# Optimization experiments

Hardware: AMD Instinct MI355X
Metric: run time of the kernel (lower is better)

## Reference

```python
import jax, jax.numpy as jnp
import numpy as np

B = 16384          # batch
D = 1024           # input_size == hidden size of each block
L = 3              # number of hidden blocks (layer_configs)
H, Q = 4, 64       # num_heads, query_size
NKV, V = 128, 256  # num_key_values, value_size  (H*V == D for residual)
OUT = 256          # out_size
EPS = 1e-5


def layernorm(x, g, b):
    m = jnp.mean(x, axis=-1, keepdims=True)
    v = jnp.mean(jnp.square(x - m), axis=-1, keepdims=True)
    return (x - m) * jax.lax.rsqrt(v + EPS) * g + b


def setup_inputs() -> dict:
    key = jax.random.key(0)
    ks = jax.random.split(key, 16)
    scale = 1e-4  # module scales Linear / out_linear weights by 0.0001 at init
    return {
        "x": jax.random.normal(ks[0], (B, D), jnp.float32),
        # per-block Linear (stacked over L identical blocks)
        "W": jax.random.normal(ks[1], (L, D, D), jnp.float32) * scale / np.sqrt(D),
        "b": jax.random.normal(ks[2], (L, D), jnp.float32) * scale,
        # MemLayer params
        "Wq": jax.random.normal(ks[3], (L, H * Q, D), jnp.float32) / np.sqrt(D),
        "keys": jax.random.normal(ks[4], (L, NKV, Q), jnp.float32),
        "values": jax.random.normal(ks[5], (L, NKV, V), jnp.float32),
        "Wout": jax.random.normal(ks[6], (L, D, H * V), jnp.float32) * scale / np.sqrt(H * V),
        # per-block LayerNorm
        "ln_g": jnp.ones((L, D), jnp.float32),
        "ln_b": jnp.zeros((L, D), jnp.float32),
        # final head: Linear(sum(layer_configs)=L*D -> OUT), LayerNorm, Sigmoid
        "Wf": jax.random.normal(ks[7], (OUT, L * D), jnp.float32) * scale / np.sqrt(L * D),
        "bf": jax.random.normal(ks[8], (OUT,), jnp.float32) * scale,
        "lnf_g": jnp.ones((OUT,), jnp.float32),
        "lnf_b": jnp.zeros((OUT,), jnp.float32),
    }


def reference(x, W, b, Wq, keys, values, Wout, ln_g, ln_b, Wf, bf, lnf_g, lnf_b):
    # Dropout layers are identity at inference.
    inv_sqrt_q = 1.0 / np.sqrt(Q).astype(np.float32)
    outs = []
    h = x
    for i in range(L):
        # Linear + ReLU
        h = jax.nn.relu(h @ W[i].T + b[i])
        # MemLayer: scores = einsum('aib,ajb->aijb').sum(-1) == q @ k^T
        q = (h @ Wq[i].T).reshape(B, H, Q)
        scores = jnp.einsum('ahq,nq->ahn', q, keys[i]) * inv_sqrt_q  # (B,H,NKV)
        attn = jax.nn.softmax(scores, axis=-1)
        # einsum('aib,ajc->aijc').mean(axis=2) == attn.sum(-1)[:,:,None] * values.mean(0)
        s = jnp.sum(attn, axis=-1)              # (B,H)
        vmean = jnp.mean(values[i], axis=0)     # (V,)
        mem = (s[:, :, None] * vmean).reshape(B, H * V)
        h = mem @ Wout[i].T + h                 # out_linear + residual
        # LayerNorm (output collected for the final concat)
        h = layernorm(h, ln_g[i], ln_b[i])
        outs.append(h)
    z = jnp.concatenate(outs, axis=-1)          # (B, L*D)
    z = z @ Wf.T + bf
    z = layernorm(z, lnf_g, lnf_b)
    return jax.nn.sigmoid(z)
```

## Files before the change

### kernel.cpp

```cpp
#include <hip/hip_runtime.h>
#include <math.h>

#define EPS 1e-5f

constexpr int Bv   = 16384;
constexpr int Dv   = 1024;
constexpr int Lv   = 3;
constexpr int NKVv = 128;
constexpr int Vv   = 256;
constexpr int OUTv = 256;
constexpr int ZLD  = Lv * Dv;

typedef short bf16x8 __attribute__((ext_vector_type(8)));
typedef float f32x4  __attribute__((ext_vector_type(4)));

using gas_t = __attribute__((address_space(1))) const void;
using las_t = __attribute__((address_space(3))) void;
#define GLD_LDS16(gp, lp) \
    __builtin_amdgcn_global_load_lds((gas_t*)(gp), (las_t*)(lp), 16, 0, 0)

static __device__ __forceinline__ ushort f2bf(float f) {
    unsigned u = __float_as_uint(f);
    u = (u + 0x7fffu + ((u >> 16) & 1u)) >> 16;
    return (ushort)u;
}
static __device__ __forceinline__ ushort f2h(float f) {
    return __builtin_bit_cast(ushort, (_Float16)f);
}
static __device__ __forceinline__ float h2f(ushort u) {
    return (float)__builtin_bit_cast(_Float16, u);
}

__global__ void vmean_kernel(const float* __restrict__ values,
                             float* __restrict__ vmean) {
    const int i = blockIdx.x, t = threadIdx.x;
    const float* vals = values + (size_t)i * NKVv * Vv;
    float s = 0.f;
    for (int n = 0; n < NKVv; ++n) s += vals[n * Vv + t];
    vmean[i * Vv + t] = s * (1.0f / NKVv);
}

__global__ void cvec_kernel(const float* __restrict__ vmean,
                            const float* __restrict__ Wout,
                            float* __restrict__ cvec) {
    const int w = threadIdx.x >> 6, lane = threadIdx.x & 63;
    const int r = blockIdx.x * 8 + w;
    const int i = r >> 10;
    const float4 mv = *(const float4*)&vmean[i * Vv + lane * 4];
    const float* row = Wout + (size_t)r * 1024;
    float acc = 0.f;
#pragma unroll
    for (int c = 0; c < 4; ++c) {
        const float4 rv = *(const float4*)&row[c * 256 + lane * 4];
        acc += mv.x * rv.x + mv.y * rv.y + mv.z * rv.z + mv.w * rv.w;
    }
#pragma unroll
    for (int o = 1; o < 64; o <<= 1) acc += __shfl_xor(acc, o, 64);
    if (lane == 0) cvec[r] = acc;
}

__global__ void wprep(const float* __restrict__ W,
                      const float* __restrict__ lng,
                      const float* __restrict__ lnb,
                      ushort* __restrict__ Wb,
                      float* __restrict__ ub, float* __restrict__ vb) {
    __shared__ float rs[8];
    const int row = blockIdx.x;
    const int i = row >> 10, n = row & 1023;
    const int t = threadIdx.x, lane = t & 63, wv = t >> 6;
    const float* Wr = W + (size_t)row * 1024;
    const float4 w4 = *(const float4*)&Wr[t * 4];
    float4 g4 = make_float4(1.f, 1.f, 1.f, 1.f);
    float4 b4 = make_float4(0.f, 0.f, 0.f, 0.f);
    if (i > 0) {
        g4 = *(const float4*)&lng[(i - 1) * 1024 + t * 4];
        b4 = *(const float4*)&lnb[(i - 1) * 1024 + t * 4];
    }
    const float s0 = w4.x * g4.x, s1 = w4.y * g4.y, s2 = w4.z * g4.z, s3 = w4.w * g4.w;
    ushort4 o = {f2bf(s0), f2bf(s1), f2bf(s2), f2bf(s3)};
    *(ushort4*)&Wb[(size_t)row * 1024 + t * 4] = o;
    float su = s0 + s1 + s2 + s3;
    float sv = w4.x * b4.x + w4.y * b4.y + w4.z * b4.z + w4.w * b4.w;
#pragma unroll
    for (int d = 1; d < 64; d <<= 1) {
        su += __shfl_xor(su, d, 64);
        sv += __shfl_xor(sv, d, 64);
    }
    if (lane == 0) { rs[wv * 2] = su; rs[wv * 2 + 1] = sv; }
    __syncthreads();
    if (t == 0 && i > 0) {
        ub[(i - 1) * 1024 + n] = rs[0] + rs[2] + rs[4] + rs[6];
        vb[(i - 1) * 1024 + n] = rs[1] + rs[3] + rs[5] + rs[7];
    }
}

__global__ void wfprep(const float* __restrict__ Wf,
                       const float* __restrict__ lng,
                       const float* __restrict__ lnb,
                       ushort* __restrict__ Wfb,
                       float* __restrict__ uf, float* __restrict__ vf) {
    __shared__ float rs[8];
    const int bid = blockIdx.x;
    const int i = bid >> 8, n = bid & 255;
    const int t = threadIdx.x, lane = t & 63, wv = t >> 6;
    const size_t base = (size_t)n * ZLD + i * 1024 + t * 4;
    const float4 w4 = *(const float4*)&Wf[base];
    const float4 g4 = *(const float4*)&lng[i * 1024 + t * 4];
    const float4 b4 = *(const float4*)&lnb[i * 1024 + t * 4];
    const float s0 = w4.x * g4.x, s1 = w4.y * g4.y, s2 = w4.z * g4.z, s3 = w4.w * g4.w;
    ushort4 o = {f2bf(s0), f2bf(s1), f2bf(s2), f2bf(s3)};
    *(ushort4*)&Wfb[base] = o;
    float su = s0 + s1 + s2 + s3;
    float sv = w4.x * b4.x + w4.y * b4.y + w4.z * b4.z + w4.w * b4.w;
#pragma unroll
    for (int d = 1; d < 64; d <<= 1) {
        su += __shfl_xor(su, d, 64);
        sv += __shfl_xor(sv, d, 64);
    }
    if (lane == 0) { rs[wv * 2] = su; rs[wv * 2 + 1] = sv; }
    __syncthreads();
    if (t == 0) {
        uf[i * 256 + n] = rs[0] + rs[2] + rs[4] + rs[6];
        vf[i * 256 + n] = rs[1] + rs[3] + rs[5] + rs[7];
    }
}

__global__ void conv_x(const float* __restrict__ x, ushort* __restrict__ z) {
    const int t = blockIdx.x * 256 + threadIdx.x;
    const int row = t >> 7, c8 = (t & 127) << 3;
    const float4 v0 = *(const float4*)&x[(size_t)row * 1024 + c8];
    const float4 v1 = *(const float4*)&x[(size_t)row * 1024 + c8 + 4];
    ushort4 o0 = {f2bf(v0.x), f2bf(v0.y), f2bf(v0.z), f2bf(v0.w)};
    ushort4 o1 = {f2bf(v1.x), f2bf(v1.y), f2bf(v1.z), f2bf(v1.w)};
    ushort* p = z + (size_t)row * ZLD + 2048 + c8;
    *(ushort4*)p       = o0;
    *(ushort4*)(p + 4) = o1;
}

#define STAGE_A(KT, BI)                                                       \
    do { _Pragma("unroll")                                                    \
        for (int j = 0; j < 4; ++j) {                                         \
            const ushort* _p = gAs + (size_t)(w * 64 + j * 16) * lda + (KT) * 32; \
            ushort* _l = As + (BI) * 8192 + (w * 64 + j * 16) * 32;           \
            GLD_LDS16(_p, _l);                                                \
        } } while (0)

#define STAGE_B(KT, BI)                                                       \
    do { _Pragma("unroll")                                                    \
        for (int j = 0; j < 4; ++j) {                                         \
            const ushort* _p = gBs + (size_t)(w * 64 + j * 16) * ldb + (KT) * 32; \
            ushort* _l = Bs + (BI) * 8192 + (w * 64 + j * 16) * 32;           \
            GLD_LDS16(_p, _l);                                                \
        } } while (0)

template<int MODE>
__global__ __launch_bounds__(256, 1)
void gemm256(const ushort* __restrict__ A, int lda,
             const ushort* __restrict__ Bw, int ldb,
             const float* __restrict__ bias,
             const float* __restrict__ cvec,
             const float* __restrict__ u_,
             const float* __restrict__ v_,
             const float2* __restrict__ pstats_in,
             float2* __restrict__ mrout,
             void* __restrict__ Cv, int ldc,
             int NT, int ksplit,
             float2* __restrict__ pstats_out) {
    __shared__ __align__(16) char smem[139264];
    ushort* As = (ushort*)smem;
    ushort* Bs = (ushort*)(smem + 49152);
    float2* mrs = (float2*)(smem + 137216);
    const int tid  = threadIdx.x;
    const int lane = tid & 63;
    const int w    = tid >> 6;
    const int wr   = w >> 1, wc = w & 1;

    const int wg  = blockIdx.x;
    int by, bx;
    if (MODE == 1) {
        const int swz = (wg & 7) * 24 + (wg >> 3);
        by = swz & 63; bx = swz >> 6;
    } else {
        const int j = wg >> 3;
        by = (wg & 7) * 8 + (j & 7);
        bx = j >> 3;
    }
    const int m0  = by * 256;
    const int n0  = (MODE == 1) ? 0 : bx * 256;
    const int koff = (MODE == 1) ? bx * ksplit : 0;

    const int schunk = ((lane & 3) ^ ((lane >> 3) & 3)) << 3;
    const ushort* gAs = A  + (size_t)(m0 + (lane >> 2)) * lda + koff + schunk;
    const ushort* gBs = Bw + (size_t)(n0 + (lane >> 2)) * ldb + koff + schunk;

    const int frow = lane & 15;
    const int ck   = (((lane >> 4) ^ ((frow >> 1) & 3))) << 3;
    const int abase = (wr * 128 + frow) * 32 + ck;
    const int bbase = (wc * 128 + frow) * 32 + ck;

    f32x4 acc[8][8] = {};

    const bool doMR = (MODE == 2) || (MODE == 1 && bx == 2);
    float2 myMR = make_float2(0.f, 0.f);
    if (doMR) {
        const float4* pp = (const float4*)(pstats_in + (((size_t)(m0 + tid)) << 3));
        float sum = 0.f, sq = 0.f;
#pragma unroll
        for (int j = 0; j < 4; ++j) {
            const float4 t4 = pp[j];
            sum += t4.x + t4.z; sq += t4.y + t4.w;
        }
        const float m = sum * (1.f / Dv);
        const float var = sq * (1.f / Dv) - m * m;
        myMR = make_float2(m, rsqrtf(var + EPS));
        if (MODE == 2) mrs[tid] = myMR;
    }
    __builtin_amdgcn_sched_barrier(0);

    STAGE_A(0, 0); STAGE_B(0, 0);
    STAGE_A(1, 1); STAGE_B(1, 1);

    for (int t = 0; t < NT; ++t) {
        if (t + 1 < NT) asm volatile("s_waitcnt vmcnt(8)" ::: "memory");
        else            asm volatile("s_waitcnt vmcnt(0)" ::: "memory");
        __builtin_amdgcn_s_barrier();
        if (t + 2 < NT) { STAGE_A(t + 2, (t + 2) % 3); STAGE_B(t + 2, (t + 2) % 3); }
        const ushort* Ab = As + (t % 3) * 8192;
        const ushort* Bb = Bs + (t % 3) * 8192;
        bf16x8 aR[8], bR[8];
#pragma unroll
        for (int mf = 0; mf < 8; ++mf) aR[mf] = *(const bf16x8*)&Ab[abase + mf * 512];
#pragma unroll
        for (int nf = 0; nf < 8; ++nf) bR[nf] = *(const bf16x8*)&Bb[bbase + nf * 512];
        __builtin_amdgcn_s_setprio(1);
#pragma unroll
        for (int mf = 0; mf < 8; ++mf)
#pragma unroll
            for (int nf = 0; nf < 8; ++nf)
                acc[mf][nf] = __builtin_amdgcn_mfma_f32_16x16x32_bf16(
                    aR[mf], bR[nf], acc[mf][nf], 0, 0, 0);
        __builtin_amdgcn_s_setprio(0);
    }

    if (doMR && (MODE == 1 || bx == 0)) mrout[m0 + tid] = myMR;

    const int lg4 = (lane >> 4) << 2;
    ushort* tile = (ushort*)(smem + 2048);
    if (MODE != 1) {
        float bsv[8], csv[8], uu[8], vv[8];
#pragma unroll
        for (int nf = 0; nf < 8; ++nf) {
            const int col = n0 + wc * 128 + nf * 16 + (lane & 15);
            bsv[nf] = bias[col];
            csv[nf] = cvec[col];
            if (MODE == 2) { uu[nf] = u_[col]; vv[nf] = v_[col]; }
        }
        __syncthreads();
#pragma unroll
        for (int mf = 0; mf < 8; ++mf)
#pragma unroll
            for (int r = 0; r < 4; ++r) {
                const int rloc = wr * 128 + mf * 16 + lg4 + r;
                float rw = 1.f, rmw = 0.f;
                if (MODE == 2) {
                    const float2 q = mrs[rloc];
                    rw = q.y; rmw = q.y * q.x;
                }
                float sum = 0.f, sq = 0.f;
#pragma unroll
                for (int nf = 0; nf < 8; ++nf) {
                    float a = acc[mf][nf][r];
                    float val;
                    if (MODE == 2)
                        val = fmaf(rw, a, fmaf(-rmw, uu[nf], vv[nf] + bsv[nf]));
                    else
                        val = a + bsv[nf];
                    val = fmaxf(val, 0.f) + csv[nf];
                    acc[mf][nf][r] = val;
                    sum += val; sq += val * val;
                }
#pragma unroll
                for (int o = 1; o < 16; o <<= 1) {
                    sum += __shfl_xor(sum, o, 64);
                    sq  += __shfl_xor(sq,  o, 64);
                }
                if ((lane & 15) == 0)
                    pstats_out[(((size_t)(m0 + rloc)) << 3) + (bx << 1) + wc] =
                        make_float2(sum, sq);
            }
#pragma unroll
        for (int mf = 0; mf < 8; ++mf)
#pragma unroll
            for (int nf = 0; nf < 8; ++nf)
#pragma unroll
                for (int r = 0; r < 4; ++r) {
                    const int rloc = wr * 128 + mf * 16 + lg4 + r;
                    const int cloc = wc * 128 + nf * 16 + (lane & 15);
                    tile[rloc * 264 + cloc] = f2bf(acc[mf][nf][r]);
                }
    } else {
        __syncthreads();
#pragma unroll
        for (int mf = 0; mf < 8; ++mf)
#pragma unroll
            for (int nf = 0; nf < 8; ++nf)
#pragma unroll
                for (int r = 0; r < 4; ++r) {
                    const int rloc = wr * 128 + mf * 16 + lg4 + r;
                    const int cloc = wc * 128 + nf * 16 + (lane & 15);
                    tile[rloc * 264 + cloc] = f2h(acc[mf][nf][r]);
                }
    }
    __syncthreads();
    ushort* C16 = (MODE == 1)
        ? ((ushort*)Cv + (size_t)bx * ((size_t)Bv * OUTv))
        : (ushort*)Cv;
    for (int c = tid; c < 256 * 32; c += 256) {
        const int row = c >> 5, ch = (c & 31) << 3;
        const bf16x8 v = *(const bf16x8*)&tile[row * 264 + ch];
        *(bf16x8*)&C16[(size_t)(m0 + row) * ldc + n0 + ch] = v;
    }
}

__global__ void ln_sig_reduce(const ushort* __restrict__ ps,
                              const float2* __restrict__ mr,
                              const float* __restrict__ uf,
                              const float* __restrict__ vf,
                              const float* __restrict__ bf_,
                              const float* __restrict__ g,
                              const float* __restrict__ bb,
                              float* __restrict__ y) {
    const int lane = threadIdx.x & 63;
    const int row  = blockIdx.x * 4 + (threadIdx.x >> 6);
    const size_t base = (size_t)row * OUTv + lane * 4;
    const size_t SP = (size_t)Bv * OUTv;
    const float2 q0 = mr[row];
    const float2 q1 = mr[Bv + row];
    const float2 q2 = mr[2 * Bv + row];
    const ushort4 a0 = *(const ushort4*)&ps[base];
    const ushort4 a1 = *(const ushort4*)&ps[base + SP];
    const ushort4 a2 = *(const ushort4*)&ps[base + 2 * SP];
    const float4 u0 = *(const float4*)&uf[lane * 4];
    const float4 u1 = *(const float4*)&uf[256 + lane * 4];
    const float4 u2 = *(const float4*)&uf[512 + lane * 4];
    const float4 f0 = *(const float4*)&vf[lane * 4];
    const float4 f1 = *(const float4*)&vf[256 + lane * 4];
    const float4 f2 = *(const float4*)&vf[512 + lane * 4];
    const float4 bv4 = *(const float4*)&bf_[lane * 4];
    const float cst_x = f0.x + f1.x + f2.x + bv4.x;
    const float cst_y = f0.y + f1.y + f2.y + bv4.y;
    const float cst_z = f0.z + f1.z + f2.z + bv4.z;
    const float cst_w = f0.w + f1.w + f2.w + bv4.w;
    const float v0 = q0.y * (h2f(a0.x) - q0.x * u0.x) + q1.y * (h2f(a1.x) - q1.x * u1.x)
                   + q2.y * (h2f(a2.x) - q2.x * u2.x) + cst_x;
    const float v1 = q0.y * (h2f(a0.y) - q0.x * u0.y) + q1.y * (h2f(a1.y) - q1.x * u1.y)
                   + q2.y * (h2f(a2.y) - q2.x * u2.y) + cst_y;
    const float v2 = q0.y * (h2f(a0.z) - q0.x * u0.z) + q1.y * (h2f(a1.z) - q1.x * u1.z)
                   + q2.y * (h2f(a2.z) - q2.x * u2.z) + cst_z;
    const float v3 = q0.y * (h2f(a0.w) - q0.x * u0.w) + q1.y * (h2f(a1.w) - q1.x * u1.w)
                   + q2.y * (h2f(a2.w) - q2.x * u2.w) + cst_w;
    float s = v0 + v1 + v2 + v3;
#pragma unroll
    for (int o = 1; o < 64; o <<= 1) s += __shfl_xor(s, o, 64);
    const float mean = s * (1.f / OUTv);
    const float d0 = v0 - mean, d1 = v1 - mean, d2 = v2 - mean, d3 = v3 - mean;
    float q = d0 * d0 + d1 * d1 + d2 * d2 + d3 * d3;
#pragma unroll
    for (int o = 1; o < 64; o <<= 1) q += __shfl_xor(q, o, 64);
    const float r = rsqrtf(q * (1.f / OUTv) + EPS);
    const float4 gg = *(const float4*)&g[lane * 4];
    const float4 bv = *(const float4*)&bb[lane * 4];
    float4 o;
    const float t0 = d0 * r * gg.x + bv.x;
    const float t1 = d1 * r * gg.y + bv.y;
    const float t2 = d2 * r * gg.z + bv.z;
    const float t3 = d3 * r * gg.w + bv.w;
    o.x = 1.f / (1.f + expf(-t0));
    o.y = 1.f / (1.f + expf(-t1));
    o.z = 1.f / (1.f + expf(-t2));
    o.w = 1.f / (1.f + expf(-t3));
    *(float4*)&y[base] = o;
}

extern "C" void kernel_launch(void* const* d_in, const int* in_sizes, int n_in,
                              void* d_out, int out_size, void* d_ws, size_t ws_size,
                              hipStream_t stream) {
    const float* x      = (const float*)d_in[0];
    const float* W      = (const float*)d_in[1];
    const float* b      = (const float*)d_in[2];
    const float* values = (const float*)d_in[5];
    const float* Wout   = (const float*)d_in[6];
    const float* ln_g   = (const float*)d_in[7];
    const float* ln_b   = (const float*)d_in[8];
    const float* Wf     = (const float*)d_in[9];
    const float* bf     = (const float*)d_in[10];
    const float* lnf_g  = (const float*)d_in[11];
    const float* lnf_b  = (const float*)d_in[12];
    float* out = (float*)d_out;

    char* ws = (char*)d_ws;
    ushort* zbuf = (ushort*)ws;
    ws += (size_t)Bv * ZLD * sizeof(ushort);
    ushort* psum = (ushort*)ws;
    ws += (size_t)3 * Bv * OUTv * sizeof(ushort);
    ushort* Wb = (ushort*)ws;
    ws += (size_t)Lv * Dv * Dv * sizeof(ushort);
    ushort* Wfb = (ushort*)ws;
    ws += (size_t)OUTv * ZLD * sizeof(ushort);
    float* cvec = (float*)ws;
    ws += (size_t)Lv * Dv * sizeof(float);
    float* vmean = (float*)ws;
    ws += (size_t)Lv * Vv * sizeof(float);
    float2* psA = (float2*)ws;
    ws += (size_t)Bv * 16 * sizeof(float2);
    float2* psB = (float2*)ws;
    ws += (size_t)Bv * 16 * sizeof(float2);
    float2* mr3 = (float2*)ws;
    ws += (size_t)3 * Bv * sizeof(float2);
    float* ub = (float*)ws; ws += 2 * Dv * sizeof(float);
    float* vb = (float*)ws; ws += 2 * Dv * sizeof(float);
    float* uf = (float*)ws; ws += 3 * OUTv * sizeof(float);
    float* vf = (float*)ws; ws += 3 * OUTv * sizeof(float);

    wprep<<<Lv * Dv, 256, 0, stream>>>(W, ln_g, ln_b, Wb, ub, vb);
    wfprep<<<3 * OUTv, 256, 0, stream>>>(Wf, ln_g, ln_b, Wfb, uf, vf);
    conv_x<<<Bv * 128 / 256, 256, 0, stream>>>(x, zbuf);
    vmean_kernel<<<Lv, 256, 0, stream>>>(values, vmean);
    cvec_kernel<<<Lv * Dv / 8, 512, 0, stream>>>(vmean, Wout, cvec);

    gemm256<0><<<dim3(256), 256, 0, stream>>>(
        zbuf + 2048, ZLD, Wb, Dv,
        b, cvec, nullptr, nullptr, nullptr, nullptr,
        (void*)(zbuf + 0), ZLD, 32, 0, psA);

    gemm256<2><<<dim3(256), 256, 0, stream>>>(
        zbuf, ZLD, Wb + (size_t)Dv * Dv, Dv,
        b + Dv, cvec + Dv, ub, vb, psA, mr3,
        (void*)(zbuf + Dv), ZLD, 32, 0, psB);

    gemm256<2><<<dim3(256), 256, 0, stream>>>(
        zbuf + Dv, ZLD, Wb + (size_t)2 * Dv * Dv, Dv,
        b + 2 * Dv, cvec + 2 * Dv, ub + Dv, vb + Dv, psB, mr3 + Bv,
        (void*)(zbuf + 2 * Dv), ZLD, 32, 0, psA);

    gemm256<1><<<dim3(192), 256, 0, stream>>>(
        zbuf, ZLD, Wfb, ZLD, nullptr, nullptr, nullptr, nullptr,
        psA, mr3 + 2 * Bv,
        (void*)psum, OUTv, 32, 1024, nullptr);

    ln_sig_reduce<<<Bv / 4, 256, 0, stream>>>(psum, mr3, uf, vf, bf,
                                              lnf_g, lnf_b, out);
}
```

Baseline: 233.2 us.

## Shrink GEMM tiles to 128x128 with double buffering and higher occupancy

Replaces the 256x256 single-workgroup-per-CU GEMM with a 128x128 tile kernel that uses double buffering instead of triple buffering and less LDS, and raises launch bounds to allow 4 workgroups per CU. Grids grow from 256/192 to 1024/768 workgroups. Per-row partial statistics are widened to 16 slots per row to match the extra column tiles. The aim is better load balance across the 256 CUs and latency hiding through occupancy, at the cost of lower arithmetic intensity per tile, more global traffic, and an extra barrier per k-step.

```diff
diff --git a/kernel.cpp b/kernel.cpp
--- a/kernel.cpp
+++ b/kernel.cpp
@@ -137,25 +137,21 @@
     *(ushort4*)(p + 4) = o1;
 }
 
-#define STAGE_A(KT, BI)                                                       \
-    do { _Pragma("unroll")                                                    \
-        for (int j = 0; j < 4; ++j) {                                         \
-            const ushort* _p = gAs + (size_t)(w * 64 + j * 16) * lda + (KT) * 32; \
-            ushort* _l = As + (BI) * 8192 + (w * 64 + j * 16) * 32;           \
-            GLD_LDS16(_p, _l);                                                \
-        } } while (0)
-
-#define STAGE_B(KT, BI)                                                       \
-    do { _Pragma("unroll")                                                    \
-        for (int j = 0; j < 4; ++j) {                                         \
-            const ushort* _p = gBs + (size_t)(w * 64 + j * 16) * ldb + (KT) * 32; \
-            ushort* _l = Bs + (BI) * 8192 + (w * 64 + j * 16) * 32;           \
-            GLD_LDS16(_p, _l);                                                \
-        } } while (0)
+#define STAGE128(KT, BI)                                                      \
+    do {                                                                      \
+        GLD_LDS16(gAs + (size_t)(w16)      * lda + (KT) * 32,                 \
+                  As + (BI) * 4096 + (w16) * 32);                             \
+        GLD_LDS16(gAs + (size_t)(w16 + 64) * lda + (KT) * 32,                 \
+                  As + (BI) * 4096 + (w16 + 64) * 32);                        \
+        GLD_LDS16(gBs + (size_t)(w16)      * ldb + (KT) * 32,                 \
+                  Bs + (BI) * 4096 + (w16) * 32);                             \
+        GLD_LDS16(gBs + (size_t)(w16 + 64) * ldb + (KT) * 32,                 \
+                  Bs + (BI) * 4096 + (w16 + 64) * 32);                        \
+    } while (0)
 
 template<int MODE>
-__global__ __launch_bounds__(256, 1)
-void gemm256(const ushort* __restrict__ A, int lda,
+__global__ __launch_bounds__(256, 4)
+void gemm128(const ushort* __restrict__ A, int lda,
              const ushort* __restrict__ Bw, int ldb,
              const float* __restrict__ bias,
              const float* __restrict__ cvec,
@@ -164,49 +160,53 @@
              const float2* __restrict__ pstats_in,
              float2* __restrict__ mrout,
              void* __restrict__ Cv, int ldc,
-             int NT, int ksplit,
+             int NT,
              float2* __restrict__ pstats_out) {
-    __shared__ __align__(16) char smem[139264];
+    __shared__ __align__(16) char smem[35840];
     ushort* As = (ushort*)smem;
-    ushort* Bs = (ushort*)(smem + 49152);
-    float2* mrs = (float2*)(smem + 137216);
+    ushort* Bs = (ushort*)(smem + 16384);
+    float2* mrs = (float2*)(smem + 34816);
     const int tid  = threadIdx.x;
     const int lane = tid & 63;
     const int w    = tid >> 6;
     const int wr   = w >> 1, wc = w & 1;
-
-    const int wg  = blockIdx.x;
-    int by, bx;
+    const int w16  = w * 16;
+
+    const int wg = blockIdx.x;
+    int by, bx, koff;
     if (MODE == 1) {
-        const int swz = (wg & 7) * 24 + (wg >> 3);
-        by = swz & 63; bx = swz >> 6;
+        const int s = wg >> 8, r = wg & 255;
+        by = r & 127; bx = r >> 7;
+        koff = s * 1024;
     } else {
         const int j = wg >> 3;
-        by = (wg & 7) * 8 + (j & 7);
-        bx = j >> 3;
-    }
-    const int m0  = by * 256;
-    const int n0  = (MODE == 1) ? 0 : bx * 256;
-    const int koff = (MODE == 1) ? bx * ksplit : 0;
+        by = (wg & 7) * 16 + (j & 15);
+        bx = j >> 4;
+        koff = 0;
+    }
+    const int m0 = by * 128;
+    const int n0 = bx * 128;
+    const int slice = (MODE == 1) ? (wg >> 8) : 0;
 
     const int schunk = ((lane & 3) ^ ((lane >> 3) & 3)) << 3;
     const ushort* gAs = A  + (size_t)(m0 + (lane >> 2)) * lda + koff + schunk;
     const ushort* gBs = Bw + (size_t)(n0 + (lane >> 2)) * ldb + koff + schunk;
 
     const int frow = lane & 15;
-    const int ck   = (((lane >> 4) ^ ((frow >> 1) & 3))) << 3;
-    const int abase = (wr * 128 + frow) * 32 + ck;
-    const int bbase = (wc * 128 + frow) * 32 + ck;
-
-    f32x4 acc[8][8] = {};
-
-    const bool doMR = (MODE == 2) || (MODE == 1 && bx == 2);
+    const int ck    = (((lane >> 4) ^ ((frow >> 1) & 3))) << 3;
+    const int abase = (wr * 64 + frow) * 32 + ck;
+    const int bbase = (wc * 64 + frow) * 32 + ck;
+
+    f32x4 acc[4][4] = {};
+    bf16x8 aR[4], bR[4];
+
+    const bool doMR = (MODE == 2) || (MODE == 1 && slice == 2);
     float2 myMR = make_float2(0.f, 0.f);
-    if (doMR) {
-        const float4* pp = (const float4*)(pstats_in + (((size_t)(m0 + tid)) << 3));
+    if (doMR && tid < 128) {
+        const float4* pp = (const float4*)(pstats_in + (((size_t)(m0 + tid)) << 4));
         float sum = 0.f, sq = 0.f;
 #pragma unroll
-        for (int j = 0; j < 4; ++j) {
+        for (int j = 0; j < 8; ++j) {
             const float4 t4 = pp[j];
             sum += t4.x + t4.z; sq += t4.y + t4.w;
         }
@@ -217,50 +217,51 @@
     }
     __builtin_amdgcn_sched_barrier(0);
 
-    STAGE_A(0, 0); STAGE_B(0, 0);
-    STAGE_A(1, 1); STAGE_B(1, 1);
+    STAGE128(0, 0);
 
     for (int t = 0; t < NT; ++t) {
-        if (t + 1 < NT) asm volatile("s_waitcnt vmcnt(8)" ::: "memory");
-        else            asm volatile("s_waitcnt vmcnt(0)" ::: "memory");
+        const int d = t & 1;
+        const bool pf = (t + 1) < NT;
         __builtin_amdgcn_s_barrier();
-        if (t + 2 < NT) { STAGE_A(t + 2, (t + 2) % 3); STAGE_B(t + 2, (t + 2) % 3); }
-        const ushort* Ab = As + (t % 3) * 8192;
-        const ushort* Bb = Bs + (t % 3) * 8192;
-        bf16x8 aR[8], bR[8];
-#pragma unroll
-        for (int mf = 0; mf < 8; ++mf) aR[mf] = *(const bf16x8*)&Ab[abase + mf * 512];
-#pragma unroll
-        for (int nf = 0; nf < 8; ++nf) bR[nf] = *(const bf16x8*)&Bb[bbase + nf * 512];
+        if (pf) STAGE128(t + 1, d ^ 1);
+        if (pf) asm volatile("s_waitcnt vmcnt(4)" ::: "memory");
+        else    asm volatile("s_waitcnt vmcnt(0)" ::: "memory");
+        __builtin_amdgcn_s_barrier();
+        const ushort* Ab = As + d * 4096;
+        const ushort* Bb = Bs + d * 4096;
+#pragma unroll
+        for (int mf = 0; mf < 4; ++mf) aR[mf] = *(const bf16x8*)&Ab[abase + mf * 512];
+#pragma unroll
+        for (int nf = 0; nf < 4; ++nf) bR[nf] = *(const bf16x8*)&Bb[bbase + nf * 512];
         __builtin_amdgcn_s_setprio(1);
 #pragma unroll
-        for (int mf = 0; mf < 8; ++mf)
-#pragma unroll
-            for (int nf = 0; nf < 8; ++nf)
+        for (int mf = 0; mf < 4; ++mf)
+#pragma unroll
+            for (int nf = 0; nf < 4; ++nf)
                 acc[mf][nf] = __builtin_amdgcn_mfma_f32_16x16x32_bf16(
                     aR[mf], bR[nf], acc[mf][nf], 0, 0, 0);
         __builtin_amdgcn_s_setprio(0);
     }
 
-    if (doMR && (MODE == 1 || bx == 0)) mrout[m0 + tid] = myMR;
+    if (doMR && tid < 128 && bx == 0) mrout[m0 + tid] = myMR;
 
     const int lg4 = (lane >> 4) << 2;
-    ushort* tile = (ushort*)(smem + 2048);
+    ushort* tile = (ushort*)smem;
     if (MODE != 1) {
-        float bsv[8], csv[8], uu[8], vv[8];
-#pragma unroll
-        for (int nf = 0; nf < 8; ++nf) {
-            const int col = n0 + wc * 128 + nf * 16 + (lane & 15);
+        float bsv[4], csv[4], uu[4], vv[4];
+#pragma unroll
+        for (int nf = 0; nf < 4; ++nf) {
+            const int col = n0 + wc * 64 + nf * 16 + (lane & 15);
             bsv[nf] = bias[col];
             csv[nf] = cvec[col];
             if (MODE == 2) { uu[nf] = u_[col]; vv[nf] = v_[col]; }
         }
         __syncthreads();
 #pragma unroll
-        for (int mf = 0; mf < 8; ++mf)
+        for (int mf = 0; mf < 4; ++mf)
 #pragma unroll
             for (int r = 0; r < 4; ++r) {
-                const int rloc = wr * 128 + mf * 16 + lg4 + r;
+                const int rloc = wr * 64 + mf * 16 + lg4 + r;
                 float rw = 1.f, rmw = 0.f;
                 if (MODE == 2) {
                     const float2 q = mrs[rloc];
@@ -268,7 +269,7 @@
                 }
                 float sum = 0.f, sq = 0.f;
 #pragma unroll
-                for (int nf = 0; nf < 8; ++nf) {
+                for (int nf = 0; nf < 4; ++nf) {
                     float a = acc[mf][nf][r];
                     float val;
                     if (MODE == 2)
@@ -285,39 +286,39 @@
                     sq  += __shfl_xor(sq,  o, 64);
                 }
                 if ((lane & 15) == 0)
-                    pstats_out[(((size_t)(m0 + rloc)) << 3) + (bx << 1) + wc] =
+                    pstats_out[(((size_t)(m0 + rloc)) << 4) + (bx << 1) + wc] =
                         make_float2(sum, sq);
             }
 #pragma unroll
-        for (int mf = 0; mf < 8; ++mf)
-#pragma unroll
-            for (int nf = 0; nf < 8; ++nf)
+        for (int mf = 0; mf < 4; ++mf)
+#pragma unroll
+            for (int nf = 0; nf < 4; ++nf)
 #pragma unroll
                 for (int r = 0; r < 4; ++r) {
-                    const int rloc = wr * 128 + mf * 16 + lg4 + r;
-                    const int cloc = wc * 128 + nf * 16 + (lane & 15);
-                    tile[rloc * 264 + cloc] = f2bf(acc[mf][nf][r]);
+                    const int rloc = wr * 64 + mf * 16 + lg4 + r;
+                    const int cloc = wc * 64 + nf * 16 + (lane & 15);
+                    tile[rloc * 136 + cloc] = f2bf(acc[mf][nf][r]);
                 }
     } else {
         __syncthreads();
 #pragma unroll
-        for (int mf = 0; mf < 8; ++mf)
-#pragma unroll
-            for (int nf = 0; nf < 8; ++nf)
+        for (int mf = 0; mf < 4; ++mf)
+#pragma unroll
+            for (int nf = 0; nf < 4; ++nf)
 #pragma unroll
                 for (int r = 0; r < 4; ++r) {
-                    const int rloc = wr * 128 + mf * 16 + lg4 + r;
-                    const int cloc = wc * 128 + nf * 16 + (lane & 15);
-                    tile[rloc * 264 + cloc] = f2h(acc[mf][nf][r]);
+                    const int rloc = wr * 64 + mf * 16 + lg4 + r;
+                    const int cloc = wc * 64 + nf * 16 + (lane & 15);
+                    tile[rloc * 136 + cloc] = f2h(acc[mf][nf][r]);
                 }
     }
     __syncthreads();
     ushort* C16 = (MODE == 1)
-        ? ((ushort*)Cv + (size_t)bx * ((size_t)Bv * OUTv))
+        ? ((ushort*)Cv + (size_t)slice * ((size_t)Bv * OUTv))
         : (ushort*)Cv;
-    for (int c = tid; c < 256 * 32; c += 256) {
-        const int row = c >> 5, ch = (c & 31) << 3;
-        const bf16x8 v = *(const bf16x8*)&tile[row * 264 + ch];
+    for (int c = tid; c < 128 * 16; c += 256) {
+        const int row = c >> 4, ch = (c & 15) << 3;
+        const bf16x8 v = *(const bf16x8*)&tile[row * 136 + ch];
         *(bf16x8*)&C16[(size_t)(m0 + row) * ldc + n0 + ch] = v;
     }
 }
@@ -428,25 +429,25 @@
     vmean_kernel<<<Lv, 256, 0, stream>>>(values, vmean);
     cvec_kernel<<<Lv * Dv / 8, 512, 0, stream>>>(vmean, Wout, cvec);
 
-    gemm256<0><<<dim3(256), 256, 0, stream>>>(
+    gemm128<0><<<dim3(1024), 256, 0, stream>>>(
         zbuf + 2048, ZLD, Wb, Dv,
         b, cvec, nullptr, nullptr, nullptr, nullptr,
-        (void*)(zbuf + 0), ZLD, 32, 0, psA);
-
-    gemm256<2><<<dim3(256), 256, 0, stream>>>(
+        (void*)(zbuf + 0), ZLD, 32, psA);
+
+    gemm128<2><<<dim3(1024), 256, 0, stream>>>(
         zbuf, ZLD, Wb + (size_t)Dv * Dv, Dv,
         b + Dv, cvec + Dv, ub, vb, psA, mr3,
-        (void*)(zbuf + Dv), ZLD, 32, 0, psB);
-
-    gemm256<2><<<dim3(256), 256, 0, stream>>>(
+        (void*)(zbuf + Dv), ZLD, 32, psB);
+
+    gemm128<2><<<dim3(1024), 256, 0, stream>>>(
         zbuf + Dv, ZLD, Wb + (size_t)2 * Dv * Dv, Dv,
         b + 2 * Dv, cvec + 2 * Dv, ub + Dv, vb + Dv, psB, mr3 + Bv,
-        (void*)(zbuf + 2 * Dv), ZLD, 32, 0, psA);
-
-    gemm256<1><<<dim3(192), 256, 0, stream>>>(
+        (void*)(zbuf + 2 * Dv), ZLD, 32, psA);
+
+    gemm128<1><<<dim3(768), 256, 0, stream>>>(
         zbuf, ZLD, Wfb, ZLD, nullptr, nullptr, nullptr, nullptr,
         psA, mr3 + 2 * Bv,
-        (void*)psum, OUTv, 32, 1024, nullptr);
+        (void*)psum, OUTv, 32, nullptr);
 
     ln_sig_reduce<<<Bv / 4, 256, 0, stream>>>(psum, mr3, uf, vf, bf,
                                               lnf_g, lnf_b, out);
```

Result: no change. 230.8 us (-1.0%).
